# Optimization experiments

Hardware: AMD Instinct MI355X
Metric: run time of the kernel (lower is better)

## Reference

```python
import jax, jax.numpy as jnp
import numpy as np

HID = 2048
HEADS = 16
HD = HID // HEADS  # 128


def setup_inputs() -> dict:
    key = jax.random.key(0)
    ks = jax.random.split(key, 9)
    s = 0.02
    return {
        "hidden_state": jax.random.normal(ks[0], (2, 2048, HID), dtype=jnp.float32),
        "Wq": jax.random.normal(ks[1], (HID, HID), dtype=jnp.float32) * s,
        "bq": jnp.zeros((HID,), dtype=jnp.float32),
        "Wk": jax.random.normal(ks[2], (HID, HD), dtype=jnp.float32) * s,
        "bk": jnp.zeros((HD,), dtype=jnp.float32),
        "Wv": jax.random.normal(ks[3], (HID, HD), dtype=jnp.float32) * s,
        "bv": jnp.zeros((HD,), dtype=jnp.float32),
        "Wo": jax.random.normal(ks[4], (HID, HID), dtype=jnp.float32) * s,
        "bo": jnp.zeros((HID,), dtype=jnp.float32),
    }


def reference(hidden_state, Wq, bq, Wk, bk, Wv, bv, Wo, bo):
    bs, seq, _ = hidden_state.shape
    # Q: [b, s, H, hd] -> per-head; K,V: single shared head [b, s, hd]
    q = (hidden_state @ Wq + bq).reshape(bs, seq, HEADS, HD)
    k = hidden_state @ Wk + bk  # [b, s, hd]
    v = hidden_state @ Wv + bv  # [b, s, hd]
    scale = 1.0 / jnp.sqrt(jnp.float32(HD))
    # scores: [b, h, s_q, s_k] against shared K head
    scores = jnp.einsum("bqhd,bkd->bhqk", q, k) * scale
    attn = jax.nn.softmax(scores, axis=-1)
    out = jnp.einsum("bhqk,bkd->bqhd", attn, v)  # [b, s, h, hd]
    out = out.reshape(bs, seq, HID)
    return out @ Wo + bo
```

## Files before the change

### kernel.cpp

```cpp
#include <hip/hip_runtime.h>
#include <math.h>

#define HIDN 2048
#define NHEADS 16
#define HDIM 128
#define SEQ 2048
#define NB 2

#define C2 0.12751744154f

typedef __bf16 bf16x8 __attribute__((ext_vector_type(8)));
typedef float f32x4 __attribute__((ext_vector_type(4)));

__device__ __forceinline__ unsigned short f32_to_bf16(float f) {
  unsigned int u = __float_as_uint(f);
  u += 0x7FFFu + ((u >> 16) & 1u);
  return (unsigned short)(u >> 16);
}

__device__ __forceinline__ unsigned pack_bf16x2(float a, float b) {
  return (unsigned)f32_to_bf16(a) | ((unsigned)f32_to_bf16(b) << 16);
}

__device__ __forceinline__ unsigned pack_bf16x2_trunc(float a, float b) {
  return __builtin_amdgcn_perm(__float_as_uint(b), __float_as_uint(a), 0x07060302u);
}

__device__ __forceinline__ void gload_lds16(const void* g, void* l) {
  __builtin_amdgcn_global_load_lds(
      (__attribute__((address_space(1))) void*)(g),
      (__attribute__((address_space(3))) void*)(l), 16, 0, 0);
}

__global__ __launch_bounds__(256) void prep(
    const float* __restrict__ hidden, unsigned short* __restrict__ hb,
    const float* __restrict__ wq, unsigned short* __restrict__ dq,
    const float* __restrict__ wo, unsigned short* __restrict__ do_,
    const float* __restrict__ wk, const float* __restrict__ wv,
    unsigned short* __restrict__ dk, unsigned short* __restrict__ dv,
    const float* __restrict__ bq, const float* __restrict__ bk,
    const float* __restrict__ bv, float* __restrict__ biasout) {
  __shared__ float tile[32][33];
  const int blk = blockIdx.x;
  const int tx = threadIdx.x & 31, ty = threadIdx.x >> 5;
  if (blk < 8192) {
    int i = blk * 256 + threadIdx.x;
    float4 v = ((const float4*)hidden)[i];
    ushort4 o;
    o.x = f32_to_bf16(v.x); o.y = f32_to_bf16(v.y);
    o.z = f32_to_bf16(v.z); o.w = f32_to_bf16(v.w);
    ((ushort4*)hb)[i] = o;
    return;
  }
  if (blk < 16384) {
    int r = blk - 8192;
    const int z = r >> 12; r &= 4095;
    const int bx = r & 63, by = r >> 6;
    const float* src = z ? wo : wq;
    unsigned short* dst = z ? do_ : dq;
    const float m = z ? 1.0f : C2;
    const int c0 = bx * 32, r0 = by * 32;
#pragma unroll
    for (int i = 0; i < 32; i += 8)
      tile[ty + i][tx] = src[(size_t)(r0 + ty + i) * 2048 + c0 + tx];
    __syncthreads();
#pragma unroll
    for (int i = 0; i < 32; i += 8)
      dst[(size_t)(c0 + ty + i) * 2048 + r0 + tx] = f32_to_bf16(tile[tx][ty + i] * m);
    return;
  }
  {
    int r = blk - 16384;
    const int z = r >> 8; r &= 255;
    const int bx = r & 3, by = r >> 2;
    const float* src = z ? wv : wk;
    unsigned short* dst = z ? dv : dk;
    const int c0 = bx * 32, r0 = by * 32;
#pragma unroll
    for (int i = 0; i < 32; i += 8)
      tile[ty + i][tx] = src[(size_t)(r0 + ty + i) * 128 + c0 + tx];
    __syncthreads();
#pragma unroll
    for (int i = 0; i < 32; i += 8)
      dst[(size_t)(c0 + ty + i) * 2048 + r0 + tx] = f32_to_bf16(tile[tx][ty + i]);
    if (z == 0) {
      int lb = by * 4 + bx;
      if (lb < 9) {
        int i = lb * 256 + threadIdx.x;
        if (i < 2304)
          biasout[i] = (i < 2048) ? bq[i] * C2
                                  : ((i < 2176) ? bk[i - 2048] : bv[i - 2176]);
      }
    }
  }
}

template <int BN, int WRITE_VT>
__global__ __launch_bounds__(256) void gemm_bt(
    const unsigned short* __restrict__ A,
    const unsigned short* __restrict__ BT,
    const float* __restrict__ bias,
    void* __restrict__ C, unsigned short* __restrict__ vtout,
    int K, int ldc, int outBf16) {
  constexpr int NT = BN / 32;
  __shared__ unsigned short As[128 * 64];
  __shared__ unsigned short Bs[BN * 64];
  const int tid = threadIdx.x;
  const int lane = tid & 63;
  const int wave = tid >> 6;
  const int wr = wave >> 1, wc = wave & 1;
  const int ml = lane & 15, quad = lane >> 4;
  const long bm = (long)blockIdx.x * 128;
  const long bn = (long)blockIdx.y * BN;

  const f32x4 zero4 = {0.f, 0.f, 0.f, 0.f};
  f32x4 acc[4][NT];
#pragma unroll
  for (int mt = 0; mt < 4; ++mt)
#pragma unroll
    for (int nt = 0; nt < NT; ++nt) acc[mt][nt] = zero4;

  const int srow = lane >> 3;
  const int scol = ((lane & 7) ^ srow) * 8;

  for (int k0 = 0; k0 < K; k0 += 64) {
    __syncthreads();
#pragma unroll
    for (int r = 0; r < 4; ++r) {
      const int rowb = r * 32 + wave * 8;
      gload_lds16(A + (bm + rowb + srow) * (long)K + k0 + scol, &As[rowb * 64]);
    }
#pragma unroll
    for (int r = 0; r < NT; ++r) {
      const int rowb = r * 32 + wave * 8;
      gload_lds16(BT + (bn + rowb + srow) * (long)K + k0 + scol, &Bs[rowb * 64]);
    }
    __syncthreads();
#pragma unroll
    for (int kk = 0; kk < 64; kk += 32) {
      const int g0 = (kk >> 3) + quad;
      bf16x8 af[4], bf[NT];
#pragma unroll
      for (int mt = 0; mt < 4; ++mt)
        af[mt] = *(const bf16x8*)&As[(wr * 64 + mt * 16 + ml) * 64 +
                                     ((g0 ^ (ml & 7)) << 3)];
#pragma unroll
      for (int nt = 0; nt < NT; ++nt)
        bf[nt] = *(const bf16x8*)&Bs[(wc * (BN / 2) + nt * 16 + ml) * 64 +
                                     ((g0 ^ (ml & 7)) << 3)];
#pragma unroll
      for (int mt = 0; mt < 4; ++mt)
#pragma unroll
        for (int nt = 0; nt < NT; ++nt)
          acc[mt][nt] = __builtin_amdgcn_mfma_f32_16x16x32_bf16(
              af[mt], bf[nt], acc[mt][nt], 0, 0, 0);
    }
  }

#pragma unroll
  for (int mt = 0; mt < 4; ++mt) {
#pragma unroll
    for (int nt = 0; nt < NT; ++nt) {
      const long col = bn + wc * (BN / 2) + nt * 16 + ml;
      const float bval = bias ? bias[col] : 0.f;
      float vv[4];
#pragma unroll
      for (int r = 0; r < 4; ++r) {
        const long row = bm + wr * 64 + mt * 16 + quad * 4 + r;
        const float v = acc[mt][nt][r] + bval;
        vv[r] = v;
        if (outBf16)
          ((unsigned short*)C)[row * ldc + col] = f32_to_bf16(v);
        else
          ((float*)C)[row * ldc + col] = v;
      }
      if (WRITE_VT) {
        if (col >= 2176) {
          const long row0 = bm + wr * 64 + mt * 16 + quad * 4;
          const int b = (int)(row0 >> 11);
          const int s0 = (int)(row0 & 2047);
          const int P = (s0 & ~63) | (((s0 >> 5) & 1) * 32 +
                                      (((s0 >> 2) & 3) * 8) +
                                      (((s0 >> 4) & 1) * 4));
          uint2 w;
          w.x = pack_bf16x2(vv[0], vv[1]);
          w.y = pack_bf16x2(vv[2], vv[3]);
          *(uint2*)&vtout[((long)b * 128 + (col - 2176)) * SEQ + P] = w;
        }
      }
    }
  }
}

__global__ __launch_bounds__(256, 2) void mqa_attn(
    const unsigned short* __restrict__ qkv,
    const unsigned short* __restrict__ vt,
    unsigned short* __restrict__ outp) {
  __shared__ unsigned short Ks[2][64 * 128];
  __shared__ unsigned short VTs[2][128 * 64];

  const int lane = threadIdx.x & 63;
  const int wave = threadIdx.x >> 6;
  const int ml = lane & 15, quad = lane >> 4;
  const int h = blockIdx.y, b = blockIdx.z;
  const long q0 = (long)blockIdx.x * 128;
  const long base = (long)b * SEQ;

  bf16x8 aq[2][4];
#pragma unroll
  for (int n = 0; n < 2; ++n) {
    const unsigned short* qrow =
        qkv + (base + q0 + wave * 32 + n * 16 + ml) * 2304 + h * 128;
#pragma unroll
    for (int ks = 0; ks < 4; ++ks)
      aq[n][ks] = *(const bf16x8*)(qrow + ks * 32 + quad * 8);
  }

  const f32x4 zero4 = {0.f, 0.f, 0.f, 0.f};
  f32x4 o[8][2];
#pragma unroll
  for (int mt2 = 0; mt2 < 8; ++mt2)
#pragma unroll
    for (int n = 0; n < 2; ++n) o[mt2][n] = zero4;
  f32x4 o9[2] = {zero4, zero4};

  bf16x8 ones_af;
  {
    union { unsigned u[4]; bf16x8 v; } cv;
    const unsigned w = (ml == 0) ? 0x3F803F80u : 0u;
    cv.u[0] = w; cv.u[1] = w; cv.u[2] = w; cv.u[3] = w;
    ones_af = cv.v;
  }

  const int srowK = lane >> 4;
  const int scolK = ((lane & 15) ^ (wave * 4 + srowK)) * 8;
  const int srowV = lane >> 3;
  const int scolV = ((lane & 7) ^ srowV) * 8;
  const unsigned short* kp = qkv + (base + srowK) * 2304 + 2048 + scolK;
  const unsigned short* vp = vt + ((long)b * 128 + srowV) * SEQ + scolV;

  auto stage = [&](int buf, int ktn) {
    const unsigned short* kpp = kp + (long)ktn * (64 * 2304);
    const unsigned short* vpp = vp + ktn * 64;
#pragma unroll
    for (int r = 0; r < 4; ++r) {
      const int rowb = r * 16 + wave * 4;
      gload_lds16(kpp + (long)rowb * 2304, &Ks[buf][rowb * 128]);
    }
#pragma unroll
    for (int r = 0; r < 4; ++r) {
      const int rowb = r * 32 + wave * 8;
      gload_lds16(vpp + (long)rowb * SEQ, &VTs[buf][rowb * 64]);
    }
  };

  stage(0, 0);

  for (int kt = 0; kt < SEQ / 64; ++kt) {
    const int cur = kt & 1;
    asm volatile("s_waitcnt vmcnt(4)" ::: "memory");
    __builtin_amdgcn_s_barrier();
    if (kt < SEQ / 64 - 1) stage(cur ^ 1, kt + 1);

    f32x4 s[4][2];
#pragma unroll
    for (int mt = 0; mt < 4; ++mt)
#pragma unroll
      for (int n = 0; n < 2; ++n) s[mt][n] = zero4;
#pragma unroll
    for (int ks = 0; ks < 4; ++ks) {
#pragma unroll
      for (int mt = 0; mt < 4; ++mt) {
        bf16x8 ak = *(const bf16x8*)&Ks[cur][(mt * 16 + ml) * 128 +
                                            (((ks * 4 + quad) ^ ml) << 3)];
#pragma unroll
        for (int n = 0; n < 2; ++n)
          s[mt][n] = __builtin_amdgcn_mfma_f32_16x16x32_bf16(
              ak, aq[n][ks], s[mt][n], 0, 0, 0);
      }
    }

    unsigned pk[2][4][2];
#pragma unroll
    for (int mt = 0; mt < 4; ++mt)
#pragma unroll
      for (int n = 0; n < 2; ++n) {
        const float p0 = __builtin_amdgcn_exp2f(s[mt][n][0]);
        const float p1 = __builtin_amdgcn_exp2f(s[mt][n][1]);
        const float p2 = __builtin_amdgcn_exp2f(s[mt][n][2]);
        const float p3 = __builtin_amdgcn_exp2f(s[mt][n][3]);
        pk[n][mt][0] = pack_bf16x2_trunc(p0, p1);
        pk[n][mt][1] = pack_bf16x2_trunc(p2, p3);
      }

    if (kt < SEQ / 64 - 1)
      asm volatile("s_waitcnt vmcnt(8)" ::: "memory");
    else
      asm volatile("s_waitcnt vmcnt(0)" ::: "memory");
    __builtin_amdgcn_s_barrier();

#pragma unroll
    for (int ks2 = 0; ks2 < 2; ++ks2) {
      bf16x8 bp[2];
#pragma unroll
      for (int n = 0; n < 2; ++n) {
        union { unsigned u[4]; bf16x8 v; } cv;
        cv.u[0] = pk[n][2 * ks2][0];
        cv.u[1] = pk[n][2 * ks2][1];
        cv.u[2] = pk[n][2 * ks2 + 1][0];
        cv.u[3] = pk[n][2 * ks2 + 1][1];
        bp[n] = cv.v;
      }
#pragma unroll
      for (int n = 0; n < 2; ++n)
        o9[n] = __builtin_amdgcn_mfma_f32_16x16x32_bf16(
            ones_af, bp[n], o9[n], 0, 0, 0);
#pragma unroll
      for (int mt2 = 0; mt2 < 8; ++mt2) {
        bf16x8 av = *(const bf16x8*)&VTs[cur][(mt2 * 16 + ml) * 64 +
                                             (((ks2 * 4 + quad) ^ (ml & 7)) << 3)];
#pragma unroll
        for (int n = 0; n < 2; ++n)
          o[mt2][n] = __builtin_amdgcn_mfma_f32_16x16x32_bf16(
              av, bp[n], o[mt2][n], 0, 0, 0);
      }
    }
  }

  float inv[2];
#pragma unroll
  for (int n = 0; n < 2; ++n)
    inv[n] = 1.f / __shfl(o9[n][0], ml);

#pragma unroll
  for (int n = 0; n < 2; ++n) {
    const long row = base + q0 + wave * 32 + n * 16 + ml;
#pragma unroll
    for (int mt2 = 0; mt2 < 8; ++mt2) {
      uint2 w;
      w.x = pack_bf16x2(o[mt2][n][0] * inv[n], o[mt2][n][1] * inv[n]);
      w.y = pack_bf16x2(o[mt2][n][2] * inv[n], o[mt2][n][3] * inv[n]);
      *(uint2*)&outp[row * HIDN + h * HDIM + mt2 * 16 + quad * 4] = w;
    }
  }
}

extern "C" void kernel_launch(void* const* d_in, const int* in_sizes, int n_in,
                              void* d_out, int out_size, void* d_ws, size_t ws_size,
                              hipStream_t stream) {
  const float* hidden = (const float*)d_in[0];
  const float* Wq = (const float*)d_in[1];
  const float* bq = (const float*)d_in[2];
  const float* Wk = (const float*)d_in[3];
  const float* bk = (const float*)d_in[4];
  const float* Wv = (const float*)d_in[5];
  const float* bv = (const float*)d_in[6];
  const float* Wo = (const float*)d_in[7];
  const float* bo = (const float*)d_in[8];
  float* out = (float*)d_out;

  char* ws = (char*)d_ws;
  const size_t MB = 1u << 20;
  unsigned short* hb    = (unsigned short*)(ws);
  unsigned short* attn  = hb;
  unsigned short* wqkvT = (unsigned short*)(ws + 16 * MB);
  unsigned short* woT   = (unsigned short*)(ws + 25 * MB);
  unsigned short* qkv   = (unsigned short*)(ws + 33 * MB);
  unsigned short* vt    = (unsigned short*)(ws + 51 * MB);
  float* biasqkv        = (float*)(ws + 52 * MB);

  prep<<<16896, 256, 0, stream>>>(hidden, hb, Wq, wqkvT, Wo, woT, Wk, Wv,
                                  wqkvT + (size_t)2048 * 2048,
                                  wqkvT + (size_t)2176 * 2048,
                                  bq, bk, bv, biasqkv);

  gemm_bt<96, 1><<<dim3(32, 24), 256, 0, stream>>>(
      hb, wqkvT, biasqkv, qkv, vt, 2048, 2304, 1);

  mqa_attn<<<dim3(SEQ / 128, NHEADS, NB), 256, 0, stream>>>(qkv, vt, attn);

  gemm_bt<128, 0><<<dim3(32, 16), 256, 0, stream>>>(
      attn, woT, bo, out, nullptr, 2048, 2048, 0);
}
```

Before: 276.2 us.

## Fuse all four kernels into one persistent kernel with grid barriers

Merges prep, the QKV GEMM, the attention and the output GEMM into a single persistent kernel of 512 blocks separated by atomic-counter grid barriers, with a memset to reset the counters. This removes the launch gaps between kernels. In exchange, the attention stage is capped at 2 blocks per CU by launch bounds, the QKV GEMM stage becomes unbalanced (half the blocks do two tiles), and the spin barriers could deadlock if not all 512 blocks are co-resident. The shared-memory size is now 64KB for every stage.

```diff
diff --git a/kernel.cpp b/kernel.cpp
--- a/kernel.cpp
+++ b/kernel.cpp
@@ -32,16 +32,26 @@
       (__attribute__((address_space(3))) void*)(l), 16, 0, 0);
 }
 
-__global__ __launch_bounds__(256) void prep(
-    const float* __restrict__ hidden, unsigned short* __restrict__ hb,
-    const float* __restrict__ wq, unsigned short* __restrict__ dq,
-    const float* __restrict__ wo, unsigned short* __restrict__ do_,
-    const float* __restrict__ wk, const float* __restrict__ wv,
-    unsigned short* __restrict__ dk, unsigned short* __restrict__ dv,
-    const float* __restrict__ bq, const float* __restrict__ bk,
-    const float* __restrict__ bv, float* __restrict__ biasout) {
-  __shared__ float tile[32][33];
-  const int blk = blockIdx.x;
+__device__ __forceinline__ void gbar(unsigned* cnt, unsigned nb) {
+  __syncthreads();
+  if (threadIdx.x == 0) {
+    __threadfence();
+    atomicAdd(cnt, 1u);
+    while (atomicAdd(cnt, 0u) < nb) __builtin_amdgcn_s_sleep(2);
+    __threadfence();
+  }
+  __syncthreads();
+}
+
+__device__ __forceinline__ void prep_blk(
+    int blk, char* smemraw,
+    const float* hidden, unsigned short* hb,
+    const float* wq, unsigned short* dq,
+    const float* wo, unsigned short* do_,
+    const float* wk, const float* wv,
+    unsigned short* dk, unsigned short* dv,
+    const float* bq, const float* bk, const float* bv, float* biasout) {
+  float (*tile)[33] = (float(*)[33])smemraw;
   const int tx = threadIdx.x & 31, ty = threadIdx.x >> 5;
   if (blk < 8192) {
     int i = blk * 256 + threadIdx.x;
@@ -96,22 +106,21 @@
 }
 
 template <int BN, int WRITE_VT>
-__global__ __launch_bounds__(256) void gemm_bt(
-    const unsigned short* __restrict__ A,
-    const unsigned short* __restrict__ BT,
-    const float* __restrict__ bias,
-    void* __restrict__ C, unsigned short* __restrict__ vtout,
+__device__ __forceinline__ void gemm_bt_blk(
+    int bxi, int byi, char* smemraw,
+    const unsigned short* A, const unsigned short* BT,
+    const float* bias, void* C, unsigned short* vtout,
     int K, int ldc, int outBf16) {
   constexpr int NT = BN / 32;
-  __shared__ unsigned short As[128 * 64];
-  __shared__ unsigned short Bs[BN * 64];
+  unsigned short* As = (unsigned short*)smemraw;
+  unsigned short* Bs = As + 128 * 64;
   const int tid = threadIdx.x;
   const int lane = tid & 63;
   const int wave = tid >> 6;
   const int wr = wave >> 1, wc = wave & 1;
   const int ml = lane & 15, quad = lane >> 4;
-  const long bm = (long)blockIdx.x * 128;
-  const long bn = (long)blockIdx.y * BN;
+  const long bm = (long)bxi * 128;
+  const long bn = (long)byi * BN;
 
   const f32x4 zero4 = {0.f, 0.f, 0.f, 0.f};
   f32x4 acc[4][NT];
@@ -192,18 +201,18 @@
   }
 }
 
-__global__ __launch_bounds__(256, 2) void mqa_attn(
+__device__ __forceinline__ void attn_blk(
+    int qblk, int h, int b, char* smemraw,
     const unsigned short* __restrict__ qkv,
     const unsigned short* __restrict__ vt,
     unsigned short* __restrict__ outp) {
-  __shared__ unsigned short Ks[2][64 * 128];
-  __shared__ unsigned short VTs[2][128 * 64];
+  unsigned short (*Ks)[64 * 128] = (unsigned short(*)[64 * 128])smemraw;
+  unsigned short (*VTs)[128 * 64] = (unsigned short(*)[128 * 64])(smemraw + 32768);
 
   const int lane = threadIdx.x & 63;
   const int wave = threadIdx.x >> 6;
   const int ml = lane & 15, quad = lane >> 4;
-  const int h = blockIdx.y, b = blockIdx.z;
-  const long q0 = (long)blockIdx.x * 128;
+  const long q0 = (long)qblk * 128;
   const long base = (long)b * SEQ;
 
   bf16x8 aq[2][4];
@@ -343,6 +352,47 @@
       *(uint2*)&outp[row * HIDN + h * HDIM + mt2 * 16 + quad * 4] = w;
     }
   }
+}
+
+__global__ __launch_bounds__(256, 2) void fused_mqa(
+    const float* __restrict__ hidden,
+    const float* __restrict__ Wq, const float* __restrict__ bq,
+    const float* __restrict__ Wk, const float* __restrict__ bk,
+    const float* __restrict__ Wv, const float* __restrict__ bv,
+    const float* __restrict__ Wo, const float* __restrict__ bo,
+    float* __restrict__ out,
+    unsigned short* __restrict__ hb, unsigned short* __restrict__ wqkvT,
+    unsigned short* __restrict__ woT, unsigned short* __restrict__ qkv,
+    unsigned short* __restrict__ vt, float* __restrict__ biasqkv,
+    unsigned* __restrict__ bar) {
+  __shared__ __align__(16) char smem[65536];
+  const int bid = blockIdx.x;
+  unsigned short* dk = wqkvT + (size_t)2048 * 2048;
+  unsigned short* dv = wqkvT + (size_t)2176 * 2048;
+  unsigned short* attn = hb;
+
+  for (int i = 0; i < 33; ++i) {
+    prep_blk(bid + 512 * i, smem, hidden, hb, Wq, wqkvT, Wo, woT, Wk, Wv,
+             dk, dv, bq, bk, bv, biasqkv);
+    __syncthreads();
+  }
+  gbar(&bar[0], 512);
+
+  gemm_bt_blk<96, 1>(bid & 31, bid >> 5, smem, hb, wqkvT, biasqkv, qkv, vt,
+                     2048, 2304, 1);
+  if (bid < 256) {
+    __syncthreads();
+    const int vb = 512 + bid;
+    gemm_bt_blk<96, 1>(vb & 31, vb >> 5, smem, hb, wqkvT, biasqkv, qkv, vt,
+                       2048, 2304, 1);
+  }
+  gbar(&bar[32], 512);
+
+  attn_blk(bid & 15, (bid >> 4) & 15, bid >> 8, smem, qkv, vt, attn);
+  gbar(&bar[64], 512);
+
+  gemm_bt_blk<128, 0>(bid & 31, bid >> 5, smem, attn, woT, bo, out, nullptr,
+                      2048, 2048, 0);
 }
 
 extern "C" void kernel_launch(void* const* d_in, const int* in_sizes, int n_in,
@@ -362,23 +412,15 @@
   char* ws = (char*)d_ws;
   const size_t MB = 1u << 20;
   unsigned short* hb    = (unsigned short*)(ws);
-  unsigned short* attn  = hb;
   unsigned short* wqkvT = (unsigned short*)(ws + 16 * MB);
   unsigned short* woT   = (unsigned short*)(ws + 25 * MB);
   unsigned short* qkv   = (unsigned short*)(ws + 33 * MB);
   unsigned short* vt    = (unsigned short*)(ws + 51 * MB);
   float* biasqkv        = (float*)(ws + 52 * MB);
-
-  prep<<<16896, 256, 0, stream>>>(hidden, hb, Wq, wqkvT, Wo, woT, Wk, Wv,
-                                  wqkvT + (size_t)2048 * 2048,
-                                  wqkvT + (size_t)2176 * 2048,
-                                  bq, bk, bv, biasqkv);
-
-  gemm_bt<96, 1><<<dim3(32, 24), 256, 0, stream>>>(
-      hb, wqkvT, biasqkv, qkv, vt, 2048, 2304, 1);
-
-  mqa_attn<<<dim3(SEQ / 128, NHEADS, NB), 256, 0, stream>>>(qkv, vt, attn);
-
-  gemm_bt<128, 0><<<dim3(32, 16), 256, 0, stream>>>(
-      attn, woT, bo, out, nullptr, 2048, 2048, 0);
-}
+  unsigned* bar         = (unsigned*)(ws + 53 * MB);
+
+  hipMemsetAsync(bar, 0, 384, stream);
+
+  fused_mqa<<<512, 256, 0, stream>>>(hidden, Wq, bq, Wk, bk, Wv, bv, Wo, bo,
+                                     out, hb, wqkvT, woT, qkv, vt, biasqkv, bar);
+}
```

Result: slower. 454.9 us (+64.7%).
